# Kernel optimization log

Hardware: AMD Instinct MI355X
Metric: run time of the kernel (lower is better)

## Reference

```python
import jax, jax.numpy as jnp
import numpy as np

B, S, D, H = 2, 2048, 1024, 16
DK = D // H  # 64
THETA = 10000.0


def _rope_tables(seq_len, d_k, theta):
    pos = jnp.arange(seq_len, dtype=jnp.float32)  # [S]
    dim = jnp.arange(0, d_k, 2, dtype=jnp.float32)  # [DK/2]
    inv_freq = 1.0 / theta ** (dim / d_k)
    angle = pos[:, None] * inv_freq[None, :]  # [S, DK/2]
    angle = jnp.repeat(angle, 2, axis=-1)  # repeat_interleave -> [S, DK]
    return jnp.cos(angle), jnp.sin(angle)


def _apply_rope(x, cos, sin):
    # x: [..., S, DK]; interleaved pair rotation
    x1 = x[..., ::2]
    x2 = x[..., 1::2]
    x_perm = jnp.stack([-x2, x1], axis=-1).reshape(x.shape)
    return x * cos + x_perm * sin


def setup_inputs() -> dict:
    key = jax.random.key(0)
    ks = jax.random.split(key, 5)
    std = np.sqrt(2.0 / (D + D)).astype(np.float32)
    return {
        "x": jax.random.normal(ks[0], (B, S, D), dtype=jnp.float32),
        "Wq": jax.random.normal(ks[1], (D, D), dtype=jnp.float32) * std,
        "Wk": jax.random.normal(ks[2], (D, D), dtype=jnp.float32) * std,
        "Wv": jax.random.normal(ks[3], (D, D), dtype=jnp.float32) * std,
        "Wo": jax.random.normal(ks[4], (D, D), dtype=jnp.float32) * std,
    }


def reference(x, Wq, Wk, Wv, Wo):
    seq_len = x.shape[-2]
    # projections: weight is [d_out, d_in], applied as x @ W^T
    def split_heads(t):
        return t.reshape(*t.shape[:-1], H, DK).swapaxes(-3, -2)  # [B, H, S, DK]

    Q = split_heads(jnp.einsum('bsd,od->bso', x, Wq))
    K = split_heads(jnp.einsum('bsd,od->bso', x, Wk))
    V = split_heads(jnp.einsum('bsd,od->bso', x, Wv))

    cos, sin = _rope_tables(seq_len, DK, THETA)  # [S, DK]
    Q = _apply_rope(Q, cos, sin)
    K = _apply_rope(K, cos, sin)

    scale = 1.0 / np.sqrt(DK).astype(np.float32)
    logits = jnp.einsum('bhnd,bhmd->bhnm', Q, K) * scale  # [B, H, S, S]
    causal = jnp.tril(jnp.ones((seq_len, seq_len), dtype=bool))
    logits = jnp.where(causal, logits, -jnp.inf)
    probs = jax.nn.softmax(logits, axis=-1)
    attn = jnp.einsum('bhnm,bhmd->bhnd', probs, V)  # [B, H, S, DK]
    attn = attn.swapaxes(-3, -2).reshape(*x.shape[:-1], D)  # [B, S, D]
    return jnp.einsum('bsd,od->bso', attn, Wo)
```

## Files before the change

### kernel.cpp

```cpp
#include <hip/hip_runtime.h>
#include <hip/hip_bf16.h>
#include <cstdint>
#include <cstddef>

#define BB 2
#define SS 2048
#define DD 1024
#define HH 16
#define DKK 64
#define MM (BB*SS)

typedef __bf16 bf16x8 __attribute__((ext_vector_type(8)));
typedef float  f32x4  __attribute__((ext_vector_type(4)));

__device__ __forceinline__ unsigned short f2bf(float f) {
    unsigned u = __float_as_uint(f);
    u += 0x7FFF + ((u >> 16) & 1);
    return (unsigned short)(u >> 16);
}

#if __has_builtin(__builtin_amdgcn_cvt_pk_bf16_f32)
typedef __bf16 bf16v2 __attribute__((ext_vector_type(2)));
__device__ __forceinline__ unsigned pk_bf16(float a, float b) {
    bf16v2 v = __builtin_amdgcn_cvt_pk_bf16_f32(a, b);
    return __builtin_bit_cast(unsigned, v);
}
#else
__device__ __forceinline__ unsigned pk_bf16(float a, float b) {
    return (unsigned)f2bf(a) | ((unsigned)f2bf(b) << 16);
}
#endif

__device__ __forceinline__ void gld_lds16(const void* g, void* l) {
    __builtin_amdgcn_global_load_lds(
        (const __attribute__((address_space(1))) unsigned int*)g,
        (__attribute__((address_space(3))) unsigned int*)l, 16, 0, 0);
}

#define WAIT_VM8() __builtin_amdgcn_s_waitcnt(0x0F78)
#define WAIT_VM4() __builtin_amdgcn_s_waitcnt(0x0F74)
#define WAIT_VM3() __builtin_amdgcn_s_waitcnt(0x0F73)
#define WAIT_VM0() __builtin_amdgcn_s_waitcnt(0x0F70)
#define BARRIER()  __builtin_amdgcn_s_barrier()

__global__ __launch_bounds__(256) void cast_all(const float* __restrict__ x,
                                                const float* __restrict__ wq,
                                                const float* __restrict__ wk,
                                                const float* __restrict__ wv,
                                                const float* __restrict__ wo,
                                                unsigned short* __restrict__ xb,
                                                unsigned short* __restrict__ wb,
                                                float2* __restrict__ tab) {
    const int bid = blockIdx.x;
    if (bid >= 8192) {
        int e = (bid - 8192) * 256 + threadIdx.x;
        int s = e >> 5, dk2 = e & 31;
        float inv_freq = exp2f(-(float)dk2 * 0.4152410118609203f);
        float sn, cs;
        __sincosf((float)s * inv_freq, &sn, &cs);
        tab[e] = make_float2(cs, sn);
        return;
    }
    int i = (bid * 256 + threadIdx.x) * 4;
    const float* src;
    unsigned short* dst;
    if (i < MM * DD) { src = x + i; dst = xb + i; }
    else {
        int e = i - MM * DD;
        int r = e >> 20;
        const float* s0 = (r == 0) ? wq : (r == 1) ? wk : (r == 2) ? wv : wo;
        src = s0 + (e & ((1 << 20) - 1));
        dst = wb + e;
    }
    float4 v = *reinterpret_cast<const float4*>(src);
    ushort4 o;
    o.x = f2bf(v.x); o.y = f2bf(v.y); o.z = f2bf(v.z); o.w = f2bf(v.w);
    *reinterpret_cast<ushort4*>(dst) = o;
}

__global__ __launch_bounds__(256, 3) void gemm_qkv(const unsigned short* __restrict__ A,
                                                   const unsigned short* __restrict__ W,
                                                   const float2* __restrict__ tab,
                                                   unsigned short* __restrict__ Qo,
                                                   unsigned short* __restrict__ Ko,
                                                   unsigned short* __restrict__ Vto) {
    __shared__ __align__(16) unsigned short A0[128 * 32], W0[128 * 32];
    __shared__ __align__(16) unsigned short A1[128 * 32], W1[128 * 32];
    const int tid  = threadIdx.x;
    const int wave = tid >> 6, lane = tid & 63;
    const int quad = lane >> 4, l16 = lane & 15;
    const int wm = wave >> 1, wn = wave & 1;
    const int m0 = blockIdx.y * 128, n0 = blockIdx.x * 128;
    const int sw3 = l16 & 3;
    const int region = n0 >> 10;

    f32x4 acc[4][4];
    for (int i = 0; i < 4; i++)
        for (int j = 0; j < 4; j++) acc[i][j] = f32x4{0.f, 0.f, 0.f, 0.f};

    auto stage = [&](int k0, unsigned short* As, unsigned short* Ws) {
        for (int c = tid; c < 512; c += 256) {
            int row = c >> 2, g = c & 3;
            int gc = ((g ^ (row & 3)) << 3);
            gld_lds16(A + (size_t)(m0 + row) * DD + k0 + gc, As + c * 8);
            gld_lds16(W + (size_t)(n0 + row) * DD + k0 + gc, Ws + c * 8);
        }
    };
    auto computeT = [&](const unsigned short* As, const unsigned short* Ws) {
        bf16x8 af[4], bfb[4];
        for (int i = 0; i < 4; i++)
            af[i] = *reinterpret_cast<const bf16x8*>(As + (wm * 64 + i * 16 + l16) * 32 + ((quad ^ sw3) << 3));
        for (int j = 0; j < 4; j++)
            bfb[j] = *reinterpret_cast<const bf16x8*>(Ws + (wn * 64 + j * 16 + l16) * 32 + ((quad ^ sw3) << 3));
        for (int i = 0; i < 4; i++)
            for (int j = 0; j < 4; j++)
                acc[i][j] = __builtin_amdgcn_mfma_f32_16x16x32_bf16(bfb[j], af[i], acc[i][j], 0, 0, 0);
    };
    auto compute = [&](const unsigned short* As, const unsigned short* Ws) {
        bf16x8 af[4], bfb[4];
        for (int i = 0; i < 4; i++)
            af[i] = *reinterpret_cast<const bf16x8*>(As + (wm * 64 + i * 16 + l16) * 32 + ((quad ^ sw3) << 3));
        for (int j = 0; j < 4; j++)
            bfb[j] = *reinterpret_cast<const bf16x8*>(Ws + (wn * 64 + j * 16 + l16) * 32 + ((quad ^ sw3) << 3));
        for (int i = 0; i < 4; i++)
            for (int j = 0; j < 4; j++)
                acc[i][j] = __builtin_amdgcn_mfma_f32_16x16x32_bf16(af[i], bfb[j], acc[i][j], 0, 0, 0);
    };

    stage(0, A0, W0);
    int k0 = 0;
    if (region < 2) {
        while (true) {
            BARRIER();
            if (k0 + 32 < DD) { stage(k0 + 32, A1, W1); WAIT_VM4(); } else WAIT_VM0();
            BARRIER();
            computeT(A0, W0);
            k0 += 32; if (k0 >= DD) break;

            BARRIER();
            if (k0 + 32 < DD) { stage(k0 + 32, A0, W0); WAIT_VM4(); } else WAIT_VM0();
            BARRIER();
            computeT(A1, W1);
            k0 += 32; if (k0 >= DD) break;
        }
        unsigned short* Co = region ? Ko : Qo;
        const float osc = (region == 0) ? 0.18033688011112042f : 1.0f;
        for (int i = 0; i < 4; i++) {
            int s = m0 + wm * 64 + i * 16 + l16;
            int b = s >> 11, srow = s & 2047;
            const float* tb = reinterpret_cast<const float*>(tab + ((size_t)srow << 5));
            for (int j = 0; j < 4; j++) {
                int nc0 = (n0 + wn * 64 + j * 16 + quad * 4) & 1023;
                int h = nc0 >> 6, dk0 = nc0 & 63;
                float4 cs = *reinterpret_cast<const float4*>(tb + dk0);
                float v0 = acc[i][j][0], v1 = acc[i][j][1];
                float v2 = acc[i][j][2], v3 = acc[i][j][3];
                float o0 = (v0 * cs.x - v1 * cs.y) * osc;
                float o1 = (v1 * cs.x + v0 * cs.y) * osc;
                float o2 = (v2 * cs.z - v3 * cs.w) * osc;
                float o3 = (v3 * cs.z + v2 * cs.w) * osc;
                uint2 w;
                w.x = pk_bf16(o0, o1);
                w.y = pk_bf16(o2, o3);
                *reinterpret_cast<uint2*>(Co + ((size_t)(b * HH + h) * SS + srow) * DKK + dk0) = w;
            }
        }
    } else {
        while (true) {
            BARRIER();
            if (k0 + 32 < DD) { stage(k0 + 32, A1, W1); WAIT_VM4(); } else WAIT_VM0();
            BARRIER();
            compute(A0, W0);
            k0 += 32; if (k0 >= DD) break;

            BARRIER();
            if (k0 + 32 < DD) { stage(k0 + 32, A0, W0); WAIT_VM4(); } else WAIT_VM0();
            BARRIER();
            compute(A1, W1);
            k0 += 32; if (k0 >= DD) break;
        }
        __syncthreads();
        unsigned short* T = A0 + wave * 1024;
        const int dkl = lane >> 2, s4 = (lane & 3) * 4;
        for (int i = 0; i < 4; i++) {
            int ms0 = m0 + wm * 64 + i * 16;
            for (int j = 0; j < 4; j++) {
                int nc0 = n0 + wn * 64 + j * 16;
                for (int r = 0; r < 4; r++)
                    T[(quad * 4 + r) * 17 + l16] = f2bf(acc[i][j][r]);
                ushort4 o;
                o.x = T[(s4 + 0) * 17 + dkl];
                o.y = T[(s4 + 1) * 17 + dkl];
                o.z = T[(s4 + 2) * 17 + dkl];
                o.w = T[(s4 + 3) * 17 + dkl];
                int nc = (nc0 + dkl) & 1023;
                int h = nc >> 6, dk = nc & 63;
                int m = ms0 + s4;
                int b = m >> 11, s = m & 2047;
                *reinterpret_cast<ushort4*>(Vto + ((size_t)((b * HH + h) * DKK + dk)) * SS + s) = o;
            }
        }
    }
}

__global__ __launch_bounds__(256, 3) void gemm_out(const unsigned short* __restrict__ A,
                                                   const unsigned short* __restrict__ W,
                                                   float* __restrict__ C) {
    __shared__ __align__(16) unsigned short A0[64 * 32], W0[128 * 32];
    __shared__ __align__(16) unsigned short A1[64 * 32], W1[128 * 32];
    const int tid  = threadIdx.x;
    const int wave = tid >> 6, lane = tid & 63;
    const int quad = lane >> 4, l16 = lane & 15;
    const int wm = wave >> 1, wn = wave & 1;
    const int m0 = blockIdx.y * 64, n0 = blockIdx.x * 128;
    const int sw3 = l16 & 3;

    f32x4 acc[2][4];
    for (int i = 0; i < 2; i++)
        for (int j = 0; j < 4; j++) acc[i][j] = f32x4{0.f, 0.f, 0.f, 0.f};

    auto stage = [&](int k0, unsigned short* As, unsigned short* Ws) {
        {
            int row = tid >> 2, g = tid & 3;
            int gc = ((g ^ (row & 3)) << 3);
            gld_lds16(A + (size_t)(m0 + row) * DD + k0 + gc, As + tid * 8);
        }
        for (int c = tid; c < 512; c += 256) {
            int row = c >> 2, g = c & 3;
            int gc = ((g ^ (row & 3)) << 3);
            gld_lds16(W + (size_t)(n0 + row) * DD + k0 + gc, Ws + c * 8);
        }
    };
    auto compute = [&](const unsigned short* As, const unsigned short* Ws) {
        bf16x8 af[2], bfb[4];
        for (int i = 0; i < 2; i++)
            af[i] = *reinterpret_cast<const bf16x8*>(As + (wm * 32 + i * 16 + l16) * 32 + ((quad ^ sw3) << 3));
        for (int j = 0; j < 4; j++)
            bfb[j] = *reinterpret_cast<const bf16x8*>(Ws + (wn * 64 + j * 16 + l16) * 32 + ((quad ^ sw3) << 3));
        for (int i = 0; i < 2; i++)
            for (int j = 0; j < 4; j++)
                acc[i][j] = __builtin_amdgcn_mfma_f32_16x16x32_bf16(bfb[j], af[i], acc[i][j], 0, 0, 0);
    };

    stage(0, A0, W0);
    int k0 = 0;
    while (true) {
        BARRIER();
        if (k0 + 32 < DD) { stage(k0 + 32, A1, W1); WAIT_VM3(); } else WAIT_VM0();
        BARRIER();
        compute(A0, W0);
        k0 += 32; if (k0 >= DD) break;

        BARRIER();
        if (k0 + 32 < DD) { stage(k0 + 32, A0, W0); WAIT_VM3(); } else WAIT_VM0();
        BARRIER();
        compute(A1, W1);
        k0 += 32; if (k0 >= DD) break;
    }

    for (int i = 0; i < 2; i++) {
        int mrow = m0 + wm * 32 + i * 16 + l16;
        for (int j = 0; j < 4; j++) {
            int ncol0 = n0 + wn * 64 + j * 16 + quad * 4;
            float4 o;
            o.x = acc[i][j][0]; o.y = acc[i][j][1];
            o.z = acc[i][j][2]; o.w = acc[i][j][3];
            *reinterpret_cast<float4*>(C + (size_t)mrow * DD + ncol0) = o;
        }
    }
}

__global__ __launch_bounds__(256, 3) void attn_kernel(const unsigned short* __restrict__ Qb,
                                                      const unsigned short* __restrict__ Kb,
                                                      const unsigned short* __restrict__ Vtb,
                                                      unsigned short* __restrict__ attn) {
    __shared__ unsigned short K0s[64 * 64], V0s[64 * 64];
    __shared__ unsigned short K1s[64 * 64], V1s[64 * 64];
    __shared__ unsigned short Ps[4][16 * 72];

    const int tid  = threadIdx.x;
    const int wave = tid >> 6, lane = tid & 63;
    const int quad = lane >> 4, l16 = lane & 15;

    const int lin = blockIdx.x;
    const int xcd = lin & 7, idx = lin >> 3;
    const int bh  = xcd * 4 + (idx & 3);
    const int tau = 31 - (idx >> 2);
    const int nST = tau + 1;

    const int swK = l16 & 7;
    const int q0r = tau * 64;

    const unsigned short* Qg = Qb  + (size_t)bh * SS * DKK;
    const unsigned short* Kg = Kb  + (size_t)bh * SS * DKK;
    const unsigned short* Vg = Vtb + (size_t)bh * DKK * SS;

    bf16x8 q0 = *reinterpret_cast<const bf16x8*>(Qg + (size_t)(q0r + wave * 16 + l16) * DKK + quad * 8);
    bf16x8 q1 = *reinterpret_cast<const bf16x8*>(Qg + (size_t)(q0r + wave * 16 + l16) * DKK + 32 + quad * 8);

    bf16x8 vone;
    for (int tt = 0; tt < 8; tt++) vone[tt] = (__bf16)1.0f;

    f32x4 ao[4], al;
    for (int j = 0; j < 4; j++) ao[j] = f32x4{0.f,0.f,0.f,0.f};
    al = f32x4{0.f,0.f,0.f,0.f};

    auto stage = [&](int s, unsigned short* Kd, unsigned short* Vd) {
        const int kv0 = s * 64;
        for (int c = tid; c < 512; c += 256) {
            int rowK = c >> 3, gK = c & 7;
            gld_lds16(Kg + (size_t)(kv0 + rowK) * DKK + ((gK ^ (rowK & 7)) << 3), Kd + c * 8);
            int rowV = c >> 3, gV = c & 7;
            gld_lds16(Vg + (size_t)rowV * SS + kv0 + ((gV ^ (rowV & 7)) << 3), Vd + c * 8);
        }
    };

    auto do_tile = [&](const unsigned short* Kd, const unsigned short* Vd, bool diag) {
        f32x4 sc[4];
        __builtin_amdgcn_s_setprio(1);
        for (int j = 0; j < 4; j++) {
            const unsigned short* kr = Kd + (j * 16 + l16) * 64;
            bf16x8 kf0 = *reinterpret_cast<const bf16x8*>(kr + ((quad ^ swK) << 3));
            bf16x8 kf1 = *reinterpret_cast<const bf16x8*>(kr + (((4 + quad) ^ swK) << 3));
            f32x4 s = f32x4{0.f, 0.f, 0.f, 0.f};
            s = __builtin_amdgcn_mfma_f32_16x16x32_bf16(q0, kf0, s, 0, 0, 0);
            s = __builtin_amdgcn_mfma_f32_16x16x32_bf16(q1, kf1, s, 0, 0, 0);
            sc[j] = s;
        }
        __builtin_amdgcn_s_setprio(0);
        if (diag) {
            for (int j = 0; j < 4; j++) {
                int lcol = j * 16 + l16;
                for (int r = 0; r < 4; r++) {
                    int lrow = wave * 16 + quad * 4 + r;
                    if (lcol > lrow) sc[j][r] = -1e30f;
                }
            }
        }
        for (int j = 0; j < 4; j++)
            for (int r = 0; r < 4; r++)
                sc[j][r] = exp2f(sc[j][r]);

        unsigned short* Pw = Ps[wave];
        for (int r = 0; r < 4; r++) {
            unsigned pA = pk_bf16(sc[0][r], sc[1][r]);
            unsigned pB = pk_bf16(sc[2][r], sc[3][r]);
            int ro = (quad * 4 + r) * 72;
            Pw[ro + l16]      = (unsigned short)pA;
            Pw[ro + 16 + l16] = (unsigned short)(pA >> 16);
            Pw[ro + 32 + l16] = (unsigned short)pB;
            Pw[ro + 48 + l16] = (unsigned short)(pB >> 16);
        }

        __builtin_amdgcn_s_setprio(1);
        for (int ko = 0; ko < 64; ko += 32) {
            bf16x8 pf = *reinterpret_cast<const bf16x8*>(Pw + l16 * 72 + ko + quad * 8);
            al = __builtin_amdgcn_mfma_f32_16x16x32_bf16(pf, vone, al, 0, 0, 0);
            int gg = (ko >> 3) + quad;
            for (int j = 0; j < 4; j++) {
                bf16x8 vf = *reinterpret_cast<const bf16x8*>(Vd + (j * 16 + l16) * 64 + ((gg ^ (l16 & 7)) << 3));
                ao[j] = __builtin_amdgcn_mfma_f32_16x16x32_bf16(pf, vf, ao[j], 0, 0, 0);
            }
        }
        __builtin_amdgcn_s_setprio(0);
    };

    stage(0, K0s, V0s);
    int s = 0;
    while (true) {
        BARRIER();
        if (s + 1 < nST) { stage(s + 1, K1s, V1s); WAIT_VM4(); } else WAIT_VM0();
        BARRIER();
        do_tile(K0s, V0s, s == tau);
        if (++s >= nST) break;

        BARRIER();
        if (s + 1 < nST) { stage(s + 1, K0s, V0s); WAIT_VM4(); } else WAIT_VM0();
        BARRIER();
        do_tile(K1s, V1s, s == tau);
        if (++s >= nST) break;
    }

    const int b = bh >> 4, h = bh & 15;
    for (int r = 0; r < 4; r++) {
        float invL = __builtin_amdgcn_rcpf(al[r]);
        int sr = q0r + wave * 16 + quad * 4 + r;
        for (int j = 0; j < 4; j++)
            attn[((size_t)(b * SS + sr)) * DD + h * DKK + j * 16 + l16] = f2bf(ao[j][r] * invL);
    }
}

extern "C" void kernel_launch(void* const* d_in, const int* in_sizes, int n_in,
                              void* d_out, int out_size, void* d_ws, size_t ws_size,
                              hipStream_t stream) {
    const float* x  = (const float*)d_in[0];
    const float* Wq = (const float*)d_in[1];
    const float* Wk = (const float*)d_in[2];
    const float* Wv = (const float*)d_in[3];
    const float* Wo = (const float*)d_in[4];

    char* ws = (char*)d_ws;
    const size_t MB = 1u << 20;
    unsigned short* xb    = (unsigned short*)(ws);
    unsigned short* wb    = (unsigned short*)(ws + 8  * MB);
    unsigned short* Qbuf  = (unsigned short*)(ws + 16 * MB);
    unsigned short* Kbuf  = (unsigned short*)(ws + 24 * MB);
    unsigned short* Vtbuf = (unsigned short*)(ws + 32 * MB);
    float2*         tab   = (float2*)(ws + 40 * MB);
    unsigned short* attnb = xb;

    cast_all<<<8448, 256, 0, stream>>>(x, Wq, Wk, Wv, Wo, xb, wb, tab);

    gemm_qkv<<<dim3(24, 32), 256, 0, stream>>>(xb, wb, tab, Qbuf, Kbuf, Vtbuf);

    attn_kernel<<<dim3(1024), 256, 0, stream>>>(Qbuf, Kbuf, Vtbuf, attnb);

    gemm_out<<<dim3(8, 64), 256, 0, stream>>>(attnb, wb + 3 * 1024 * 1024, (float*)d_out);
}
```

Baseline: 179.9 us.

## Use 128-row query tiles with 8 waves sharing each K/V tile in attention

The attention kernel now runs 512 threads per block, so 8 waves cover 128 query rows and share each staged 64-row K/V tile. This halves the number of blocks and the K/V global-to-LDS traffic per query row. The query-tile order is remapped to interleave long and short causal blocks for load balance. On the last tile only the upper four waves do work, and the larger block raises register and occupancy pressure.

```diff
diff --git a/kernel.cpp b/kernel.cpp
--- a/kernel.cpp
+++ b/kernel.cpp
@@ -40,6 +40,7 @@
 #define WAIT_VM8() __builtin_amdgcn_s_waitcnt(0x0F78)
 #define WAIT_VM4() __builtin_amdgcn_s_waitcnt(0x0F74)
 #define WAIT_VM3() __builtin_amdgcn_s_waitcnt(0x0F73)
+#define WAIT_VM2() __builtin_amdgcn_s_waitcnt(0x0F72)
 #define WAIT_VM0() __builtin_amdgcn_s_waitcnt(0x0F70)
 #define BARRIER()  __builtin_amdgcn_s_barrier()
 
@@ -270,13 +271,13 @@
     }
 }
 
-__global__ __launch_bounds__(256, 3) void attn_kernel(const unsigned short* __restrict__ Qb,
+__global__ __launch_bounds__(512, 6) void attn_kernel(const unsigned short* __restrict__ Qb,
                                                       const unsigned short* __restrict__ Kb,
                                                       const unsigned short* __restrict__ Vtb,
                                                       unsigned short* __restrict__ attn) {
     __shared__ unsigned short K0s[64 * 64], V0s[64 * 64];
     __shared__ unsigned short K1s[64 * 64], V1s[64 * 64];
-    __shared__ unsigned short Ps[4][16 * 72];
+    __shared__ unsigned short Ps[8][16 * 72];
 
     const int tid  = threadIdx.x;
     const int wave = tid >> 6, lane = tid & 63;
@@ -285,11 +286,12 @@
     const int lin = blockIdx.x;
     const int xcd = lin & 7, idx = lin >> 3;
     const int bh  = xcd * 4 + (idx & 3);
-    const int tau = 31 - (idx >> 2);
-    const int nST = tau + 1;
+    const int g   = idx >> 2;
+    const int tau = (g < 8) ? (15 - g) : (g - 8);
+    const int nST = 2 * tau + 2;
 
     const int swK = l16 & 7;
-    const int q0r = tau * 64;
+    const int q0r = tau * 128;
 
     const unsigned short* Qg = Qb  + (size_t)bh * SS * DKK;
     const unsigned short* Kg = Kb  + (size_t)bh * SS * DKK;
@@ -307,15 +309,13 @@
 
     auto stage = [&](int s, unsigned short* Kd, unsigned short* Vd) {
         const int kv0 = s * 64;
-        for (int c = tid; c < 512; c += 256) {
-            int rowK = c >> 3, gK = c & 7;
-            gld_lds16(Kg + (size_t)(kv0 + rowK) * DKK + ((gK ^ (rowK & 7)) << 3), Kd + c * 8);
-            int rowV = c >> 3, gV = c & 7;
-            gld_lds16(Vg + (size_t)rowV * SS + kv0 + ((gV ^ (rowV & 7)) << 3), Vd + c * 8);
-        }
-    };
-
-    auto do_tile = [&](const unsigned short* Kd, const unsigned short* Vd, bool diag) {
+        const int row = tid >> 3, gi = tid & 7;
+        gld_lds16(Kg + (size_t)(kv0 + row) * DKK + ((gi ^ (row & 7)) << 3), Kd + tid * 8);
+        gld_lds16(Vg + (size_t)row * SS + kv0 + ((gi ^ (row & 7)) << 3), Vd + tid * 8);
+    };
+
+    auto do_tile = [&](const unsigned short* Kd, const unsigned short* Vd,
+                       bool diag, int doff) {
         f32x4 sc[4];
         __builtin_amdgcn_s_setprio(1);
         for (int j = 0; j < 4; j++) {
@@ -330,7 +330,7 @@
         __builtin_amdgcn_s_setprio(0);
         if (diag) {
             for (int j = 0; j < 4; j++) {
-                int lcol = j * 16 + l16;
+                int lcol = doff + j * 16 + l16;
                 for (int r = 0; r < 4; r++) {
                     int lrow = wave * 16 + quad * 4 + r;
                     if (lcol > lrow) sc[j][r] = -1e30f;
@@ -365,19 +365,26 @@
         __builtin_amdgcn_s_setprio(0);
     };
 
+    auto step = [&](const unsigned short* Kd, const unsigned short* Vd, int s) {
+        int rel = s - 2 * tau;
+        if (rel < 0)       do_tile(Kd, Vd, false, 0);
+        else if (rel == 0) do_tile(Kd, Vd, true, 0);
+        else if (wave >= 4) do_tile(Kd, Vd, true, 64);
+    };
+
     stage(0, K0s, V0s);
     int s = 0;
     while (true) {
         BARRIER();
-        if (s + 1 < nST) { stage(s + 1, K1s, V1s); WAIT_VM4(); } else WAIT_VM0();
-        BARRIER();
-        do_tile(K0s, V0s, s == tau);
+        if (s + 1 < nST) { stage(s + 1, K1s, V1s); WAIT_VM2(); } else WAIT_VM0();
+        BARRIER();
+        step(K0s, V0s, s);
         if (++s >= nST) break;
 
         BARRIER();
-        if (s + 1 < nST) { stage(s + 1, K0s, V0s); WAIT_VM4(); } else WAIT_VM0();
-        BARRIER();
-        do_tile(K1s, V1s, s == tau);
+        if (s + 1 < nST) { stage(s + 1, K0s, V0s); WAIT_VM2(); } else WAIT_VM0();
+        BARRIER();
+        step(K1s, V1s, s);
         if (++s >= nST) break;
     }
 
@@ -413,7 +420,7 @@
 
     gemm_qkv<<<dim3(24, 32), 256, 0, stream>>>(xb, wb, tab, Qbuf, Kbuf, Vtbuf);
 
-    attn_kernel<<<dim3(1024), 256, 0, stream>>>(Qbuf, Kbuf, Vtbuf, attnb);
+    attn_kernel<<<dim3(512), 512, 0, stream>>>(Qbuf, Kbuf, Vtbuf, attnb);
 
     gemm_out<<<dim3(8, 64), 256, 0, stream>>>(attnb, wb + 3 * 1024 * 1024, (float*)d_out);
 }
```

Measured after the change: 191.8 us. +6.7%, slower.
